# Kernel optimization log

Hardware: AMD Instinct MI355X
Metric: run time of the kernel (lower is better)

The kernel has to match this reference:

```python
import jax, jax.numpy as jnp
import numpy as np

# Keras LSTM with recurrent_activation='tanh' (non-standard: gates i,f,o use tanh, not sigmoid).
# mask_zero=True: timesteps where token==0 are skipped (state carried through).
# Dropout is inference-mode (disabled). return_sequences=False -> final_output == state_h.

B, S, E, U_DIM, V = 32, 512, 512, 1024, 32000


def setup_inputs() -> dict:
    key = jax.random.key(0)
    k1, k2, k3, k4 = jax.random.split(key, 4)
    tokens = jax.random.randint(k1, (B, S), 0, V, dtype=jnp.int64)
    emb = jax.random.normal(k2, (V, E), dtype=jnp.float32) * 0.02
    W = jax.random.normal(k3, (E, 4 * U_DIM), dtype=jnp.float32) * (1.0 / np.sqrt(E))
    Ur = jax.random.normal(k4, (U_DIM, 4 * U_DIM), dtype=jnp.float32) * (1.0 / np.sqrt(U_DIM))
    b = jnp.zeros((4 * U_DIM,), dtype=jnp.float32)
    return {"tokens": tokens, "emb": emb, "W": W, "U": Ur, "b": b}


def _lstm_scan(tokens, emb, W, U, b):
    x = emb[tokens]                      # [B,S,E] embedding lookup
    mask = (tokens != 0)                 # [B,S] mask_zero=True
    xW = jnp.einsum('bse,eg->bsg', x, W) + b   # precompute input gate pre-activations [B,S,4U]
    u = U.shape[0]

    def step(carry, inp):
        h, c = carry
        xw_t, m_t = inp                  # [B,4U], [B]
        z = xw_t + h @ U                 # [B,4U]
        zi, zf, zg, zo = jnp.split(z, 4, axis=-1)
        i = jnp.tanh(zi)                 # recurrent_activation='tanh'
        f = jnp.tanh(zf)
        g = jnp.tanh(zg)
        o = jnp.tanh(zo)
        c_new = f * c + i * g
        h_new = o * jnp.tanh(c_new)
        m = m_t[:, None]
        h = jnp.where(m, h_new, h)       # masked steps carry state
        c = jnp.where(m, c_new, c)
        return (h, c), None

    h0 = jnp.zeros((tokens.shape[0], u), dtype=xW.dtype)
    c0 = jnp.zeros_like(h0)
    (h, c), _ = jax.lax.scan(step, (h0, c0),
                             (jnp.swapaxes(xW, 0, 1), jnp.swapaxes(mask, 0, 1)))
    return h, c


def reference(tokens, emb, W, U, b):
    h, c = _lstm_scan(tokens, emb, W, U, b)
    # (final_output, [state_h, state_c]); final_output == state_h when return_sequences=False
    return (h, h, c)
```

## Files before the change

### kernel.cpp

```cpp
#include <hip/hip_runtime.h>
#include <hip/hip_bf16.h>

#define B_    32
#define S_    512
#define E_    512
#define H_    1024
#define G4_   4096
#define NSB_  32
#define NGB_  224
#define HPAD_ 1048

typedef __attribute__((ext_vector_type(8))) short short8;
typedef __attribute__((ext_vector_type(4))) float f32x4;
typedef unsigned long long u64;

__device__ __forceinline__ float bf2f(ushort u) {
    union { unsigned u32; float f; } cv; cv.u32 = ((unsigned)u) << 16; return cv.f;
}
__device__ __forceinline__ ushort f2bf(float f) {
    union { float f; unsigned u; } cv; cv.f = f;
    unsigned u = cv.u;
    u += 0x7FFFu + ((u >> 16) & 1u);
    return (ushort)(u >> 16);
}
__device__ __forceinline__ float tanh_fast(float x) {
    float e = __builtin_amdgcn_exp2f(x * 2.885390081777927f);
    return 1.0f - 2.0f * __builtin_amdgcn_rcpf(e + 1.0f);
}
__device__ __forceinline__ float sel4(int s, float a0, float a1, float a2, float a3) {
    return (s & 2) ? ((s & 1) ? a3 : a2) : ((s & 1) ? a1 : a0);
}

__global__ void init_kernel(const int* __restrict__ tokens, u64* hA, unsigned* cnt,
                            unsigned* __restrict__ m32) {
    int i = blockIdx.x * 256 + threadIdx.x;
    hA[i] = 0ull; hA[i + 4096] = 0ull;
    if (i < 128) cnt[i] = 0u;
    if (i < 512) {
        unsigned m = 0;
        for (int b = 0; b < 32; ++b)
            m |= (tokens[b * S_ + i] != 0 ? 1u : 0u) << b;
        m32[i] = m;
    }
}

__global__ void transpose_w_kernel(const float* __restrict__ src, ushort* __restrict__ dst) {
    __shared__ float tile[32][33];
    int kx = blockIdx.y * 32;
    int nx = blockIdx.x * 32;
    int c  = threadIdx.x & 31;
    int r0 = threadIdx.x >> 5;
    for (int rr = r0; rr < 32; rr += 8)
        tile[rr][c] = src[(size_t)(kx + rr) * G4_ + nx + c];
    __syncthreads();
    for (int rr = r0; rr < 32; rr += 8)
        dst[(size_t)(nx + rr) * E_ + kx + c] = f2bf(tile[c][rr]);
}

__global__ void transpose_u_kernel(const float* __restrict__ src, unsigned* __restrict__ dst) {
    __shared__ float tile[32][33];
    int kx = blockIdx.y * 32;
    int nx = blockIdx.x * 32;
    int c  = threadIdx.x & 31;
    int r0 = threadIdx.x >> 5;
    for (int rr = r0; rr < 32; rr += 8)
        tile[rr][c] = src[(size_t)(kx + rr) * G4_ + nx + c];
    __syncthreads();
    int r  = threadIdx.x >> 3;
    int c3 = threadIdx.x & 7;
    int n  = nx + r;
    int np = (n & 1023) * 4 + (n >> 10);
    float v0 = tile[c3 * 4 + 0][r] * 64.0f;
    float v1 = tile[c3 * 4 + 1][r] * 64.0f;
    float v2 = tile[c3 * 4 + 2][r] * 64.0f;
    float v3 = tile[c3 * 4 + 3][r] * 64.0f;
    int pk = __builtin_amdgcn_cvt_pk_fp8_f32(v0, v1, 0, false);
    pk     = __builtin_amdgcn_cvt_pk_fp8_f32(v2, v3, pk, true);
    dst[((size_t)np * H_ + kx + c3 * 4) >> 2] = (unsigned)pk;
}

__global__ __launch_bounds__(512, 1) void mono_kernel(
    const unsigned char* __restrict__ UT,
    ushort* xWT,
    const unsigned* __restrict__ m32,
    u64* hA, u64* hB,
    unsigned* cnt,
    float* __restrict__ out,
    const int* __restrict__ tokens,
    const float* __restrict__ emb,
    const ushort* __restrict__ WT,
    const float* __restrict__ bias) {
    __shared__ u64 smem[4192];

    const int tid  = threadIdx.x;
    const int lane = tid & 63;
    const int w    = tid >> 6;
    const int lr = lane & 15, lq = lane >> 4;

    if (blockIdx.x >= NSB_) {
        const int blkg = blockIdx.x - NSB_;
        u64* Cs = smem;
        for (int u = blkg; u < 4096; u += NGB_) {
            const int mb = u >> 5, jb = u & 31;
            const int t    = mb * 4 + (w >> 1);
            const int brow = (w & 1) * 16 + lr;
            const int tok  = tokens[brow * S_ + t];
            const float* arow = emb + (size_t)tok * E_;

            f32x4 acc[8] = {{0,0,0,0},{0,0,0,0},{0,0,0,0},{0,0,0,0},
                            {0,0,0,0},{0,0,0,0},{0,0,0,0},{0,0,0,0}};
            #pragma unroll 2
            for (int ks = 0; ks < E_ / 32; ++ks) {
                const float* ap = arow + ks * 32 + lq * 8;
                float4 a0 = *reinterpret_cast<const float4*>(ap);
                float4 a1 = *reinterpret_cast<const float4*>(ap + 4);
                short8 af;
                af[0] = (short)f2bf(a0.x); af[1] = (short)f2bf(a0.y);
                af[2] = (short)f2bf(a0.z); af[3] = (short)f2bf(a0.w);
                af[4] = (short)f2bf(a1.x); af[5] = (short)f2bf(a1.y);
                af[6] = (short)f2bf(a1.z); af[7] = (short)f2bf(a1.w);
                #pragma unroll
                for (int s = 0; s < 4; ++s)
                    #pragma unroll
                    for (int h = 0; h < 2; ++h) {
                        const ushort* bp = WT + (size_t)(s * 1024 + jb * 32 + h * 16 + lr) * E_;
                        short8 bf = *reinterpret_cast<const short8*>(bp + ks * 32 + lq * 8);
                        acc[s * 2 + h] = __builtin_amdgcn_mfma_f32_16x16x32_bf16(af, bf, acc[s * 2 + h], 0, 0, 0);
                    }
            }
            #pragma unroll
            for (int s = 0; s < 4; ++s)
                #pragma unroll
                for (int h = 0; h < 2; ++h) {
                    int n = s * 1024 + jb * 32 + h * 16 + lr;
                    float bv = bias[n];
                    u64 pk = 0;
                    #pragma unroll
                    for (int r = 0; r < 4; ++r)
                        pk |= (u64)f2bf(acc[s * 2 + h][r] + bv) << (16 * r);
                    int npl = (h * 16 + lr) * 4 + s;
                    Cs[((size_t)(w >> 1) * 128 + npl) * 8 + (w & 1) * 4 + lq] = pk;
                }
            __syncthreads();
            #pragma unroll
            for (int i = 0; i < 8; ++i) {
                int e   = tid + i * 512;
                int tp  = e >> 10;
                int rem = e & 1023;
                u64* dst = (u64*)(xWT + ((size_t)(mb * 4 + tp) * G4_ + jb * 128) * B_) + rem;
                __hip_atomic_store(dst, Cs[e], __ATOMIC_RELAXED, __HIP_MEMORY_SCOPE_AGENT);
            }
            __syncthreads();
            if (tid == 0)
                __hip_atomic_fetch_add(&cnt[mb], 1u, __ATOMIC_RELAXED, __HIP_MEMORY_SCOPE_AGENT);
        }
        return;
    }

    unsigned char* Hs = (unsigned char*)smem;
    const int blk  = blockIdx.x;
    const int m0 = (w & 1) * 16;
    const int n0 = blk * 128 + (w >> 1) * 32;
    const int c0 = n0 + lr;
    const int c1 = n0 + 16 + lr;
    const int g  = lr & 3;
    const int cb = blk * 8 + (w >> 1) * 2;

    u64 ub0[32], ub1[32];
    #pragma unroll
    for (int ks = 0; ks < 32; ++ks) {
        ub0[ks] = *reinterpret_cast<const u64*>(UT + (size_t)c0 * H_ + ks * 32 + lq * 8);
        ub1[ks] = *reinterpret_cast<const u64*>(UT + (size_t)c1 * H_ + ks * 32 + lq * 8);
    }
    #pragma unroll
    for (int ks = 0; ks < 32; ++ks) {
        asm volatile("" : "+v"(ub0[ks]));
        asm volatile("" : "+v"(ub1[ks]));
    }

    float creg0[4] = {0,0,0,0}, hreg0[4] = {0,0,0,0};
    float creg1[4] = {0,0,0,0}, hreg1[4] = {0,0,0,0};

    const u64* hcur = hA;
    u64*       hnxt = hB;

    while (__hip_atomic_load(&cnt[0], __ATOMIC_RELAXED, __HIP_MEMORY_SCOPE_AGENT) < 32u)
        __builtin_amdgcn_s_sleep(8);
    asm volatile("" ::: "memory");
    u64 xwv0 = *reinterpret_cast<const u64*>(xWT + ((size_t)0 * G4_ + c0) * B_ + m0 + lq * 4);
    u64 xwv1 = *reinterpret_cast<const u64*>(xWT + ((size_t)0 * G4_ + c1) * B_ + m0 + lq * 4);
    unsigned mask = m32[0];
    int mb_conf = 1;
    unsigned cv = __hip_atomic_load(&cnt[1], __ATOMIC_RELAXED, __HIP_MEMORY_SCOPE_AGENT);

    for (int t = 0; t < S_; ++t) {
        {
            const unsigned tv = (unsigned)t;
            u64 hv[16];
            for (;;) {
                #pragma unroll
                for (int i = 0; i < 16; ++i)
                    hv[i] = __hip_atomic_load(hcur + tid + i * 512,
                                              __ATOMIC_RELAXED, __HIP_MEMORY_SCOPE_AGENT);
                unsigned bad = 0u;
                #pragma unroll
                for (int i = 0; i < 16; ++i)
                    bad |= ((unsigned)(hv[i] >> 32)) ^ tv;
                if (__all(bad == 0u)) break;
                __builtin_amdgcn_s_sleep(1);
            }
            #pragma unroll
            for (int i = 0; i < 16; ++i) {
                int e = tid + i * 512, row = e >> 8, kc = e & 255;
                *reinterpret_cast<unsigned*>(&Hs[row * HPAD_ + kc * 4]) = (unsigned)hv[i];
            }
        }
        __syncthreads();

        f32x4 acc0 = {0,0,0,0}, acc1 = {0,0,0,0};
        #pragma unroll
        for (int ks = 0; ks < 32; ++ks) {
            u64 af = *reinterpret_cast<const u64*>(&Hs[(m0 + lr) * HPAD_ + ks * 32 + lq * 8]);
            acc0 = __builtin_amdgcn_mfma_f32_16x16x32_fp8_fp8((long)af, (long)ub0[ks], acc0, 0, 0, 0);
            acc1 = __builtin_amdgcn_mfma_f32_16x16x32_fp8_fp8((long)af, (long)ub1[ks], acc1, 0, 0, 0);
        }

        const u64 tagw = (u64)(unsigned)(t + 1) << 32;
        const bool notlast = (t < S_ - 1);
        #pragma unroll
        for (int r = 0; r < 4; ++r) {
            bool mbk = (mask >> (m0 + lq * 4 + r)) & 1;
            {
                float z  = acc0[r] * (1.0f / 16384.0f) + bf2f((ushort)(xwv0 >> (16 * r)));
                float tg = tanh_fast(z);
                float x1 = __shfl_xor(tg, 1, 64);
                float x2 = __shfl_xor(tg, 2, 64);
                float x3 = __shfl_xor(tg, 3, 64);
                float tI = sel4(g,     tg, x1, x2, x3);
                float tF = sel4(g ^ 1, tg, x1, x2, x3);
                float tG = sel4(g ^ 2, tg, x1, x2, x3);
                float tO = sel4(g ^ 3, tg, x1, x2, x3);
                float cn = tF * creg0[r] + tI * tG;
                float hn = tO * tanh_fast(cn);
                if (mbk) { creg0[r] = cn; hreg0[r] = hn; }
            }
            {
                float z  = acc1[r] * (1.0f / 16384.0f) + bf2f((ushort)(xwv1 >> (16 * r)));
                float tg = tanh_fast(z);
                float x1 = __shfl_xor(tg, 1, 64);
                float x2 = __shfl_xor(tg, 2, 64);
                float x3 = __shfl_xor(tg, 3, 64);
                float tI = sel4(g,     tg, x1, x2, x3);
                float tF = sel4(g ^ 1, tg, x1, x2, x3);
                float tG = sel4(g ^ 2, tg, x1, x2, x3);
                float tO = sel4(g ^ 3, tg, x1, x2, x3);
                float cn = tF * creg1[r] + tI * tG;
                float hn = tO * tanh_fast(cn);
                if (mbk) { creg1[r] = cn; hreg1[r] = hn; }
            }
            if (notlast) {
                float a0 = hreg0[r] * 256.0f;
                float b0 = __shfl_xor(a0, 4, 64);
                float cc0 = __shfl_xor(a0, 8, 64);
                float d0 = __shfl_xor(a0, 12, 64);
                int pk0 = __builtin_amdgcn_cvt_pk_fp8_f32(a0, b0, 0, false);
                pk0     = __builtin_amdgcn_cvt_pk_fp8_f32(cc0, d0, pk0, true);
                float a1 = hreg1[r] * 256.0f;
                float b1 = __shfl_xor(a1, 4, 64);
                float cc1 = __shfl_xor(a1, 8, 64);
                float d1 = __shfl_xor(a1, 12, 64);
                int pk1 = __builtin_amdgcn_cvt_pk_fp8_f32(a1, b1, 0, false);
                pk1     = __builtin_amdgcn_cvt_pk_fp8_f32(cc1, d1, pk1, true);
                if (lr == 0) {
                    int row = m0 + lq * 4 + r;
                    __hip_atomic_store(hnxt + row * 256 + cb,     (u64)(unsigned)pk0 | tagw,
                                       __ATOMIC_RELAXED, __HIP_MEMORY_SCOPE_AGENT);
                    __hip_atomic_store(hnxt + row * 256 + cb + 1, (u64)(unsigned)pk1 | tagw,
                                       __ATOMIC_RELAXED, __HIP_MEMORY_SCOPE_AGENT);
                }
            }
        }

        if (notlast) {
            int mbn = (t + 1) >> 2;
            if (mbn >= mb_conf) {
                while (cv < 32u) {
                    __builtin_amdgcn_s_sleep(4);
                    cv = __hip_atomic_load(&cnt[mbn], __ATOMIC_RELAXED, __HIP_MEMORY_SCOPE_AGENT);
                }
                mb_conf = mbn + 1;
                int nx = mbn + 1 < 128 ? mbn + 1 : 127;
                cv = __hip_atomic_load(&cnt[nx], __ATOMIC_RELAXED, __HIP_MEMORY_SCOPE_AGENT);
                asm volatile("" ::: "memory");
            }
            xwv0 = *reinterpret_cast<const u64*>(xWT + ((size_t)(t + 1) * G4_ + c0) * B_ + m0 + lq * 4);
            xwv1 = *reinterpret_cast<const u64*>(xWT + ((size_t)(t + 1) * G4_ + c1) * B_ + m0 + lq * 4);
            mask = m32[t + 1];
            const u64* tsw = hcur; hcur = hnxt; hnxt = (u64*)tsw;
        } else {
            if (g == 0) {
                int j0 = c0 >> 2, j1 = c1 >> 2;
                #pragma unroll
                for (int r = 0; r < 4; ++r) {
                    int row = m0 + lq * 4 + r;
                    out[row * H_ + j0]               = hreg0[r];
                    out[B_ * H_ + row * H_ + j0]     = hreg0[r];
                    out[2 * B_ * H_ + row * H_ + j0] = creg0[r];
                    out[row * H_ + j1]               = hreg1[r];
                    out[B_ * H_ + row * H_ + j1]     = hreg1[r];
                    out[2 * B_ * H_ + row * H_ + j1] = creg1[r];
                }
            }
        }
    }
}

extern "C" void kernel_launch(void* const* d_in, const int* in_sizes, int n_in,
                              void* d_out, int out_size, void* d_ws, size_t ws_size,
                              hipStream_t stream) {
    (void)in_sizes; (void)n_in; (void)out_size; (void)ws_size;
    const int*   tokens = (const int*)  d_in[0];
    const float* emb    = (const float*)d_in[1];
    const float* W      = (const float*)d_in[2];
    const float* U      = (const float*)d_in[3];
    const float* bias   = (const float*)d_in[4];

    char* ws = (char*)d_ws;
    ushort*        WT   = (ushort*)ws;
    unsigned char* UT   = (unsigned char*)(ws + (4u << 20));
    ushort*        xWT  = (ushort*)(ws + (8u << 20));
    u64*           hA   = (u64*)(ws + (136u << 20));
    u64*           hB   = hA + 8192;
    unsigned*      m32  = (unsigned*)(hB + 8192);
    unsigned*      cnt  = m32 + 512;

    init_kernel<<<16, 256, 0, stream>>>(tokens, hA, cnt, m32);
    transpose_w_kernel<<<dim3(G4_ / 32, E_ / 32), 256, 0, stream>>>(W, WT);
    transpose_u_kernel<<<dim3(G4_ / 32, H_ / 32), 256, 0, stream>>>(U, (unsigned*)UT);
    mono_kernel<<<NSB_ + NGB_, 512, 0, stream>>>(UT, xWT, m32, hA, hB, cnt, (float*)d_out,
                                                 tokens, emb, WT, bias);
}
```

Before: 2.257 ms.

## Swap MFMA operands so each lane holds all four gates, dropping gate shuffles

The recurrent MFMA now takes U as the A operand and h as B, so the four gate columns of one hidden unit land in one lane's accumulator. This removes the per-step cross-lane shuffles and selects that gathered the i/f/g/o gates, and halves the U register footprint per wave (one 16-column strip per wave instead of two). The xW precompute now writes a [t][b][j] layout of packed 4-gate u64s directly with atomic stores, dropping the shared-memory staging and its extra barrier. Each wave now reads two h row tiles from LDS per k-step, and the fp8 packing of h needs a different shuffle pattern.

```diff
diff --git a/kernel.cpp b/kernel.cpp
--- a/kernel.cpp
+++ b/kernel.cpp
@@ -26,9 +26,6 @@
 __device__ __forceinline__ float tanh_fast(float x) {
     float e = __builtin_amdgcn_exp2f(x * 2.885390081777927f);
     return 1.0f - 2.0f * __builtin_amdgcn_rcpf(e + 1.0f);
-}
-__device__ __forceinline__ float sel4(int s, float a0, float a1, float a2, float a3) {
-    return (s & 2) ? ((s & 1) ? a3 : a2) : ((s & 1) ? a1 : a0);
 }
 
 __global__ void init_kernel(const int* __restrict__ tokens, u64* hA, unsigned* cnt,
@@ -81,7 +78,7 @@
 
 __global__ __launch_bounds__(512, 1) void mono_kernel(
     const unsigned char* __restrict__ UT,
-    ushort* xWT,
+    u64* xWT,
     const unsigned* __restrict__ m32,
     u64* hA, u64* hB,
     unsigned* cnt,
@@ -99,7 +96,6 @@
 
     if (blockIdx.x >= NSB_) {
         const int blkg = blockIdx.x - NSB_;
-        u64* Cs = smem;
         for (int u = blkg; u < 4096; u += NGB_) {
             const int mb = u >> 5, jb = u & 31;
             const int t    = mb * 4 + (w >> 1);
@@ -129,26 +125,21 @@
                     }
             }
             #pragma unroll
-            for (int s = 0; s < 4; ++s)
-                #pragma unroll
-                for (int h = 0; h < 2; ++h) {
-                    int n = s * 1024 + jb * 32 + h * 16 + lr;
-                    float bv = bias[n];
+            for (int h = 0; h < 2; ++h) {
+                int j = jb * 32 + h * 16 + lr;
+                float bv[4];
+                #pragma unroll
+                for (int s = 0; s < 4; ++s) bv[s] = bias[s * 1024 + j];
+                #pragma unroll
+                for (int r = 0; r < 4; ++r) {
+                    int b = (w & 1) * 16 + lq * 4 + r;
                     u64 pk = 0;
                     #pragma unroll
-                    for (int r = 0; r < 4; ++r)
-                        pk |= (u64)f2bf(acc[s * 2 + h][r] + bv) << (16 * r);
-                    int npl = (h * 16 + lr) * 4 + s;
-                    Cs[((size_t)(w >> 1) * 128 + npl) * 8 + (w & 1) * 4 + lq] = pk;
+                    for (int s = 0; s < 4; ++s)
+                        pk |= (u64)f2bf(acc[s * 2 + h][r] + bv[s]) << (16 * s);
+                    __hip_atomic_store(xWT + ((size_t)t * B_ + b) * 1024 + j, pk,
+                                       __ATOMIC_RELAXED, __HIP_MEMORY_SCOPE_AGENT);
                 }
-            __syncthreads();
-            #pragma unroll
-            for (int i = 0; i < 8; ++i) {
-                int e   = tid + i * 512;
-                int tp  = e >> 10;
-                int rem = e & 1023;
-                u64* dst = (u64*)(xWT + ((size_t)(mb * 4 + tp) * G4_ + jb * 128) * B_) + rem;
-                __hip_atomic_store(dst, Cs[e], __ATOMIC_RELAXED, __HIP_MEMORY_SCOPE_AGENT);
             }
             __syncthreads();
             if (tid == 0)
@@ -159,27 +150,21 @@
 
     unsigned char* Hs = (unsigned char*)smem;
     const int blk  = blockIdx.x;
-    const int m0 = (w & 1) * 16;
-    const int n0 = blk * 128 + (w >> 1) * 32;
-    const int c0 = n0 + lr;
-    const int c1 = n0 + 16 + lr;
-    const int g  = lr & 3;
-    const int cb = blk * 8 + (w >> 1) * 2;
-
-    u64 ub0[32], ub1[32];
+    const int nb  = blk * 128 + w * 16;
+    const int jw  = nb >> 2;
+    const int jme = jw + lq;
+    const int cw  = blk * 8 + w;
+
+    u64 ub[32];
     #pragma unroll
-    for (int ks = 0; ks < 32; ++ks) {
-        ub0[ks] = *reinterpret_cast<const u64*>(UT + (size_t)c0 * H_ + ks * 32 + lq * 8);
-        ub1[ks] = *reinterpret_cast<const u64*>(UT + (size_t)c1 * H_ + ks * 32 + lq * 8);
-    }
+    for (int ks = 0; ks < 32; ++ks)
+        ub[ks] = *reinterpret_cast<const u64*>(UT + (size_t)(nb + lr) * H_ + ks * 32 + lq * 8);
     #pragma unroll
-    for (int ks = 0; ks < 32; ++ks) {
-        asm volatile("" : "+v"(ub0[ks]));
-        asm volatile("" : "+v"(ub1[ks]));
-    }
-
-    float creg0[4] = {0,0,0,0}, hreg0[4] = {0,0,0,0};
-    float creg1[4] = {0,0,0,0}, hreg1[4] = {0,0,0,0};
+    for (int ks = 0; ks < 32; ++ks)
+        asm volatile("" : "+v"(ub[ks]));
+
+    float c0 = 0.f, h0 = 0.f;
+    float c1 = 0.f, h1 = 0.f;
 
     const u64* hcur = hA;
     u64*       hnxt = hB;
@@ -187,8 +172,8 @@
     while (__hip_atomic_load(&cnt[0], __ATOMIC_RELAXED, __HIP_MEMORY_SCOPE_AGENT) < 32u)
         __builtin_amdgcn_s_sleep(8);
     asm volatile("" ::: "memory");
-    u64 xwv0 = *reinterpret_cast<const u64*>(xWT + ((size_t)0 * G4_ + c0) * B_ + m0 + lq * 4);
-    u64 xwv1 = *reinterpret_cast<const u64*>(xWT + ((size_t)0 * G4_ + c1) * B_ + m0 + lq * 4);
+    u64 xwv0 = xWT[((size_t)0 * B_ + lr) * 1024 + jme];
+    u64 xwv1 = xWT[((size_t)0 * B_ + 16 + lr) * 1024 + jme];
     unsigned mask = m32[0];
     int mb_conf = 1;
     unsigned cv = __hip_atomic_load(&cnt[1], __ATOMIC_RELAXED, __HIP_MEMORY_SCOPE_AGENT);
@@ -220,68 +205,54 @@
         f32x4 acc0 = {0,0,0,0}, acc1 = {0,0,0,0};
         #pragma unroll
         for (int ks = 0; ks < 32; ++ks) {
-            u64 af = *reinterpret_cast<const u64*>(&Hs[(m0 + lr) * HPAD_ + ks * 32 + lq * 8]);
-            acc0 = __builtin_amdgcn_mfma_f32_16x16x32_fp8_fp8((long)af, (long)ub0[ks], acc0, 0, 0, 0);
-            acc1 = __builtin_amdgcn_mfma_f32_16x16x32_fp8_fp8((long)af, (long)ub1[ks], acc1, 0, 0, 0);
-        }
-
-        const u64 tagw = (u64)(unsigned)(t + 1) << 32;
+            u64 bf0 = *reinterpret_cast<const u64*>(&Hs[lr * HPAD_ + ks * 32 + lq * 8]);
+            u64 bf1 = *reinterpret_cast<const u64*>(&Hs[(16 + lr) * HPAD_ + ks * 32 + lq * 8]);
+            acc0 = __builtin_amdgcn_mfma_f32_16x16x32_fp8_fp8((long)ub[ks], (long)bf0, acc0, 0, 0, 0);
+            acc1 = __builtin_amdgcn_mfma_f32_16x16x32_fp8_fp8((long)ub[ks], (long)bf1, acc1, 0, 0, 0);
+        }
+
         const bool notlast = (t < S_ - 1);
-        #pragma unroll
-        for (int r = 0; r < 4; ++r) {
-            bool mbk = (mask >> (m0 + lq * 4 + r)) & 1;
+        {
+            float ti = tanh_fast(acc0[0] * (1.0f / 16384.0f) + bf2f((ushort)(xwv0)));
+            float tf = tanh_fast(acc0[1] * (1.0f / 16384.0f) + bf2f((ushort)(xwv0 >> 16)));
+            float tg = tanh_fast(acc0[2] * (1.0f / 16384.0f) + bf2f((ushort)(xwv0 >> 32)));
+            float to = tanh_fast(acc0[3] * (1.0f / 16384.0f) + bf2f((ushort)(xwv0 >> 48)));
+            float cn = tf * c0 + ti * tg;
+            float hn = to * tanh_fast(cn);
+            if ((mask >> lr) & 1) { c0 = cn; h0 = hn; }
+        }
+        {
+            float ti = tanh_fast(acc1[0] * (1.0f / 16384.0f) + bf2f((ushort)(xwv1)));
+            float tf = tanh_fast(acc1[1] * (1.0f / 16384.0f) + bf2f((ushort)(xwv1 >> 16)));
+            float tg = tanh_fast(acc1[2] * (1.0f / 16384.0f) + bf2f((ushort)(xwv1 >> 32)));
+            float to = tanh_fast(acc1[3] * (1.0f / 16384.0f) + bf2f((ushort)(xwv1 >> 48)));
+            float cn = tf * c1 + ti * tg;
+            float hn = to * tanh_fast(cn);
+            if ((mask >> (16 + lr)) & 1) { c1 = cn; h1 = hn; }
+        }
+
+        if (notlast) {
+            const u64 tagw = (u64)(unsigned)(t + 1) << 32;
             {
-                float z  = acc0[r] * (1.0f / 16384.0f) + bf2f((ushort)(xwv0 >> (16 * r)));
-                float tg = tanh_fast(z);
-                float x1 = __shfl_xor(tg, 1, 64);
-                float x2 = __shfl_xor(tg, 2, 64);
-                float x3 = __shfl_xor(tg, 3, 64);
-                float tI = sel4(g,     tg, x1, x2, x3);
-                float tF = sel4(g ^ 1, tg, x1, x2, x3);
-                float tG = sel4(g ^ 2, tg, x1, x2, x3);
-                float tO = sel4(g ^ 3, tg, x1, x2, x3);
-                float cn = tF * creg0[r] + tI * tG;
-                float hn = tO * tanh_fast(cn);
-                if (mbk) { creg0[r] = cn; hreg0[r] = hn; }
+                float a = h0 * 256.0f;
+                float bx = __shfl_xor(a, 16, 64);
+                int lo = __builtin_amdgcn_cvt_pk_fp8_f32(a, bx, 0, false);
+                int hi = __shfl_xor(lo, 32, 64);
+                unsigned pk = ((unsigned)lo & 0xFFFFu) | ((unsigned)hi << 16);
+                if (lq == 0)
+                    __hip_atomic_store(hnxt + lr * 256 + cw, (u64)pk | tagw,
+                                       __ATOMIC_RELAXED, __HIP_MEMORY_SCOPE_AGENT);
             }
             {
-                float z  = acc1[r] * (1.0f / 16384.0f) + bf2f((ushort)(xwv1 >> (16 * r)));
-                float tg = tanh_fast(z);
-                float x1 = __shfl_xor(tg, 1, 64);
-                float x2 = __shfl_xor(tg, 2, 64);
-                float x3 = __shfl_xor(tg, 3, 64);
-                float tI = sel4(g,     tg, x1, x2, x3);
-                float tF = sel4(g ^ 1, tg, x1, x2, x3);
-                float tG = sel4(g ^ 2, tg, x1, x2, x3);
-                float tO = sel4(g ^ 3, tg, x1, x2, x3);
-                float cn = tF * creg1[r] + tI * tG;
-                float hn = tO * tanh_fast(cn);
-                if (mbk) { creg1[r] = cn; hreg1[r] = hn; }
-            }
-            if (notlast) {
-                float a0 = hreg0[r] * 256.0f;
-                float b0 = __shfl_xor(a0, 4, 64);
-                float cc0 = __shfl_xor(a0, 8, 64);
-                float d0 = __shfl_xor(a0, 12, 64);
-                int pk0 = __builtin_amdgcn_cvt_pk_fp8_f32(a0, b0, 0, false);
-                pk0     = __builtin_amdgcn_cvt_pk_fp8_f32(cc0, d0, pk0, true);
-                float a1 = hreg1[r] * 256.0f;
-                float b1 = __shfl_xor(a1, 4, 64);
-                float cc1 = __shfl_xor(a1, 8, 64);
-                float d1 = __shfl_xor(a1, 12, 64);
-                int pk1 = __builtin_amdgcn_cvt_pk_fp8_f32(a1, b1, 0, false);
-                pk1     = __builtin_amdgcn_cvt_pk_fp8_f32(cc1, d1, pk1, true);
-                if (lr == 0) {
-                    int row = m0 + lq * 4 + r;
-                    __hip_atomic_store(hnxt + row * 256 + cb,     (u64)(unsigned)pk0 | tagw,
+                float a = h1 * 256.0f;
+                float bx = __shfl_xor(a, 16, 64);
+                int lo = __builtin_amdgcn_cvt_pk_fp8_f32(a, bx, 0, false);
+                int hi = __shfl_xor(lo, 32, 64);
+                unsigned pk = ((unsigned)lo & 0xFFFFu) | ((unsigned)hi << 16);
+                if (lq == 0)
+                    __hip_atomic_store(hnxt + (16 + lr) * 256 + cw, (u64)pk | tagw,
                                        __ATOMIC_RELAXED, __HIP_MEMORY_SCOPE_AGENT);
-                    __hip_atomic_store(hnxt + row * 256 + cb + 1, (u64)(unsigned)pk1 | tagw,
-                                       __ATOMIC_RELAXED, __HIP_MEMORY_SCOPE_AGENT);
-                }
-            }
-        }
-
-        if (notlast) {
+            }
             int mbn = (t + 1) >> 2;
             if (mbn >= mb_conf) {
                 while (cv < 32u) {
@@ -293,24 +264,17 @@
                 cv = __hip_atomic_load(&cnt[nx], __ATOMIC_RELAXED, __HIP_MEMORY_SCOPE_AGENT);
                 asm volatile("" ::: "memory");
             }
-            xwv0 = *reinterpret_cast<const u64*>(xWT + ((size_t)(t + 1) * G4_ + c0) * B_ + m0 + lq * 4);
-            xwv1 = *reinterpret_cast<const u64*>(xWT + ((size_t)(t + 1) * G4_ + c1) * B_ + m0 + lq * 4);
+            xwv0 = xWT[((size_t)(t + 1) * B_ + lr) * 1024 + jme];
+            xwv1 = xWT[((size_t)(t + 1) * B_ + 16 + lr) * 1024 + jme];
             mask = m32[t + 1];
             const u64* tsw = hcur; hcur = hnxt; hnxt = (u64*)tsw;
         } else {
-            if (g == 0) {
-                int j0 = c0 >> 2, j1 = c1 >> 2;
-                #pragma unroll
-                for (int r = 0; r < 4; ++r) {
-                    int row = m0 + lq * 4 + r;
-                    out[row * H_ + j0]               = hreg0[r];
-                    out[B_ * H_ + row * H_ + j0]     = hreg0[r];
-                    out[2 * B_ * H_ + row * H_ + j0] = creg0[r];
-                    out[row * H_ + j1]               = hreg1[r];
-                    out[B_ * H_ + row * H_ + j1]     = hreg1[r];
-                    out[2 * B_ * H_ + row * H_ + j1] = creg1[r];
-                }
-            }
+            out[lr * H_ + jme]                      = h0;
+            out[B_ * H_ + lr * H_ + jme]            = h0;
+            out[2 * B_ * H_ + lr * H_ + jme]        = c0;
+            out[(16 + lr) * H_ + jme]               = h1;
+            out[B_ * H_ + (16 + lr) * H_ + jme]     = h1;
+            out[2 * B_ * H_ + (16 + lr) * H_ + jme] = c1;
         }
     }
 }
@@ -328,7 +292,7 @@
     char* ws = (char*)d_ws;
     ushort*        WT   = (ushort*)ws;
     unsigned char* UT   = (unsigned char*)(ws + (4u << 20));
-    ushort*        xWT  = (ushort*)(ws + (8u << 20));
+    u64*           xWT  = (u64*)(ws + (8u << 20));
     u64*           hA   = (u64*)(ws + (136u << 20));
     u64*           hB   = hA + 8192;
     unsigned*      m32  = (unsigned*)(hB + 8192);
```

Result: slower. 2.505 ms (+11.0%).
